# Kernel tuning notes

Hardware: AMD Instinct MI355X
Metric: run time of the kernel (lower is better)

Reference implementation:

```python
import jax, jax.numpy as jnp
import numpy as np

B = 256        # batch size
D = 256        # feature dim
N = 100000     # memory bank size (num pseudo classes)
TEMP = 0.07    # SCT_Memory temperature


def setup_inputs() -> dict:
    key = jax.random.key(0)
    k1, k2, k3 = jax.random.split(key, 3)
    inputs = jax.random.normal(k1, (B, D), dtype=jnp.float32)
    # ReID features are L2-normalized before hitting the memory
    inputs = inputs / jnp.linalg.norm(inputs, axis=1, keepdims=True)
    indexes = jax.random.randint(k2, (B,), 0, N, dtype=jnp.int32)
    features = jax.random.normal(k3, (N, D), dtype=jnp.float32)
    features = features / jnp.linalg.norm(features, axis=1, keepdims=True)
    return {"inputs": inputs, "indexes": indexes, "features": features,
            "momentum": 0.2}


def reference(inputs, indexes, features, momentum):
    # ExemplarMemory.forward: outputs = inputs.mm(features.t())
    # SCT_Memory then scales by 1/temp to form cluster_score.
    out = jnp.matmul(inputs, features.T)  # [B, N]
    return out / TEMP
```

## Files before the change

kernel.cpp:

```cpp
#include <hip/hip_runtime.h>
#include <hip/hip_bf16.h>


typedef __attribute__((ext_vector_type(8))) __bf16 bf16x8;
typedef __attribute__((ext_vector_type(4))) float  floatx4;
typedef __attribute__((ext_vector_type(4))) unsigned int uint4v;

#define NB 100000
#define KD 256
#define BN 64
#define NTILES 1563
#define GRID 256
#define LDS_STRIDE 132

union FragCast { uint4v u; bf16x8 f; };

__device__ __forceinline__ unsigned pk(float a, float b) {
  __hip_bfloat162 h = __float22bfloat162_rn(float2{a, b});
  union { __hip_bfloat162 h2; unsigned u; } c; c.h2 = h; return c.u;
}

__global__ __launch_bounds__(1024, 4)
void sct_gemm(const float* __restrict__ inputs,
              const float* __restrict__ features,
              float* __restrict__ out) {
  __shared__ unsigned lds[BN * LDS_STRIDE];

  const int tid  = threadIdx.x;
  const int ws   = tid >> 6;
  const int lane = tid & 63;
  const int quad = lane >> 4;
  const int l16  = lane & 15;

  const int b = blockIdx.x;
  const int ntiles = (NTILES - b + GRID - 1) / GRID;

  const int srow0 = tid >> 5,            sck0 = tid & 31;
  const int srow1 = (1024 + tid) >> 5,   sck1 = tid & 31;

  float4 pf0a, pf0b, pf1a, pf1b;
  {
    const int n0 = b * BN;
    pf0a = pf0b = pf1a = pf1b = make_float4(0.f, 0.f, 0.f, 0.f);
    if (n0 + srow0 < NB) {
      const float4* p = (const float4*)(features + (size_t)(n0 + srow0) * KD + sck0 * 8);
      pf0a = p[0]; pf0b = p[1];
    }
    if (n0 + srow1 < NB) {
      const float4* p = (const float4*)(features + (size_t)(n0 + srow1) * KD + sck1 * 8);
      pf1a = p[0]; pf1b = p[1];
    }
  }

  const float scale = 1.0f / 0.07f;
  bf16x8 afrag[8];
  {
    const float* arow = inputs + (ws * 16 + l16) * KD + quad * 8;
    #pragma unroll
    for (int t = 0; t < 8; ++t) {
      const float4* p = (const float4*)(arow + t * 32);
      const float4 a0 = p[0], a1 = p[1];
      FragCast fc;
      fc.u.x = pk(a0.x * scale, a0.y * scale);
      fc.u.y = pk(a0.z * scale, a0.w * scale);
      fc.u.z = pk(a1.x * scale, a1.y * scale);
      fc.u.w = pk(a1.z * scale, a1.w * scale);
      afrag[t] = fc.f;
    }
  }

  const unsigned obase = (unsigned)((ws * 16 + quad * 4) * NB + l16);

  for (int it = 0; it < ntiles; ++it) {
    const int n0 = (b + it * GRID) * BN;

    __syncthreads();

    {
      uint4v w;
      w.x = pk(pf0a.x, pf0a.y); w.y = pk(pf0a.z, pf0a.w);
      w.z = pk(pf0b.x, pf0b.y); w.w = pk(pf0b.z, pf0b.w);
      *(uint4v*)&lds[srow0 * LDS_STRIDE + sck0 * 4] = w;
      w.x = pk(pf1a.x, pf1a.y); w.y = pk(pf1a.z, pf1a.w);
      w.z = pk(pf1b.x, pf1b.y); w.w = pk(pf1b.z, pf1b.w);
      *(uint4v*)&lds[srow1 * LDS_STRIDE + sck1 * 4] = w;
    }
    __syncthreads();

    if (it + 1 < ntiles) {
      const int nn0 = (b + (it + 1) * GRID) * BN;
      pf0a = pf0b = pf1a = pf1b = make_float4(0.f, 0.f, 0.f, 0.f);
      if (nn0 + srow0 < NB) {
        const float4* p = (const float4*)(features + (size_t)(nn0 + srow0) * KD + sck0 * 8);
        pf0a = p[0]; pf0b = p[1];
      }
      if (nn0 + srow1 < NB) {
        const float4* p = (const float4*)(features + (size_t)(nn0 + srow1) * KD + sck1 * 8);
        pf1a = p[0]; pf1b = p[1];
      }
    }

    floatx4 acc[4];
    #pragma unroll
    for (int nt = 0; nt < 4; ++nt) acc[nt] = floatx4{0.f, 0.f, 0.f, 0.f};

    #pragma unroll
    for (int t = 0; t < 8; ++t) {
      #pragma unroll
      for (int nt = 0; nt < 4; ++nt) {
        FragCast fc;
        fc.u = *(const uint4v*)&lds[(nt * 16 + l16) * LDS_STRIDE + t * 16 + quad * 4];
        acc[nt] = __builtin_amdgcn_mfma_f32_16x16x32_bf16(afrag[t], fc.f, acc[nt], 0, 0, 0);
      }
    }

    #pragma unroll
    for (int nt = 0; nt < 4; ++nt) {
      const int n = n0 + nt * 16 + l16;
      if (n < NB) {
        const unsigned col = obase + (unsigned)(n0 + nt * 16);
        #pragma unroll
        for (int r = 0; r < 4; ++r)
          out[col + (unsigned)(r * NB)] = acc[nt][r];
      }
    }
  }
}

extern "C" void kernel_launch(void* const* d_in, const int* in_sizes, int n_in,
                              void* d_out, int out_size, void* d_ws, size_t ws_size,
                              hipStream_t stream) {
  const float* inputs   = (const float*)d_in[0];
  const float* features = (const float*)d_in[2];
  float* out = (float*)d_out;

  sct_gemm<<<GRID, 1024, 0, stream>>>(inputs, features, out);
}
```

Measured before the change: 200.2 us.

## Stage A in swizzled LDS, stream B straight from global per wave

Moves the scaled bf16 input matrix (half of the batch rows per block) into XOR-swizzled LDS. Each wave now loads its own 16-row feature slice directly from global into MFMA fragments, with no LDS staging of features and no per-tile block barriers. The grid doubles to 512 blocks, each wave group handles 16-column tasks strided across the bank, and launch bounds are raised to 8. This removes the syncthreads and the LDS round trip for B, but each feature row is now read from global twice (once per batch half) and the direct loads have no explicit prefetch.

```diff
diff --git a/kernel.cpp b/kernel.cpp
--- a/kernel.cpp
+++ b/kernel.cpp
@@ -6,12 +6,11 @@
 typedef __attribute__((ext_vector_type(4))) float  floatx4;
 typedef __attribute__((ext_vector_type(4))) unsigned int uint4v;
 
-#define NB 100000
-#define KD 256
-#define BN 64
-#define NTILES 1563
-#define GRID 256
-#define LDS_STRIDE 132
+#define NB    100000
+#define KD    256
+#define NSUB  6250
+#define NGRP  512
+#define GRIDB 512
 
 union FragCast { uint4v u; bf16x8 f; };
 
@@ -20,110 +19,73 @@
   union { __hip_bfloat162 h2; unsigned u; } c; c.h2 = h; return c.u;
 }
 
-__global__ __launch_bounds__(1024, 4)
+__global__ __launch_bounds__(1024, 8)
 void sct_gemm(const float* __restrict__ inputs,
               const float* __restrict__ features,
               float* __restrict__ out) {
-  __shared__ unsigned lds[BN * LDS_STRIDE];
+  __shared__ unsigned ldsA[128 * 128];
 
   const int tid  = threadIdx.x;
-  const int ws   = tid >> 6;
+  const int b    = blockIdx.x;
+  const int h    = b & 1;
+  const int wv   = tid >> 6;
   const int lane = tid & 63;
   const int quad = lane >> 4;
   const int l16  = lane & 15;
+  const float scale = 1.0f / 0.07f;
 
-  const int b = blockIdx.x;
-  const int ntiles = (NTILES - b + GRID - 1) / GRID;
+  #pragma unroll
+  for (int i = 0; i < 4; ++i) {
+    const int c  = i * 1024 + tid;
+    const int r  = c >> 5;
+    const int ck = c & 31;
+    const float4* p = (const float4*)(inputs + (size_t)(h * 128 + r) * KD + ck * 8);
+    const float4 a0 = p[0], a1 = p[1];
+    uint4v w;
+    w.x = pk(a0.x * scale, a0.y * scale);
+    w.y = pk(a0.z * scale, a0.w * scale);
+    w.z = pk(a1.x * scale, a1.y * scale);
+    w.w = pk(a1.z * scale, a1.w * scale);
+    *(uint4v*)&ldsA[r * 128 + ((ck * 4) ^ ((r & 7) * 16))] = w;
+  }
+  __syncthreads();
 
-  const int srow0 = tid >> 5,            sck0 = tid & 31;
-  const int srow1 = (1024 + tid) >> 5,   sck1 = tid & 31;
+  const int mb = wv & 7;
+  const int g  = ((b >> 1) << 1) + (wv >> 3);
 
-  float4 pf0a, pf0b, pf1a, pf1b;
-  {
-    const int n0 = b * BN;
-    pf0a = pf0b = pf1a = pf1b = make_float4(0.f, 0.f, 0.f, 0.f);
-    if (n0 + srow0 < NB) {
-      const float4* p = (const float4*)(features + (size_t)(n0 + srow0) * KD + sck0 * 8);
-      pf0a = p[0]; pf0b = p[1];
-    }
-    if (n0 + srow1 < NB) {
-      const float4* p = (const float4*)(features + (size_t)(n0 + srow1) * KD + sck1 * 8);
-      pf1a = p[0]; pf1b = p[1];
-    }
-  }
+  const unsigned aBase = (unsigned)((mb * 16 + l16) * 128 + quad * 4);
+  const unsigned aSwz  = (unsigned)((l16 & 7) * 16);
 
-  const float scale = 1.0f / 0.07f;
-  bf16x8 afrag[8];
-  {
-    const float* arow = inputs + (ws * 16 + l16) * KD + quad * 8;
-    #pragma unroll
-    for (int t = 0; t < 8; ++t) {
-      const float4* p = (const float4*)(arow + t * 32);
-      const float4 a0 = p[0], a1 = p[1];
-      FragCast fc;
-      fc.u.x = pk(a0.x * scale, a0.y * scale);
-      fc.u.y = pk(a0.z * scale, a0.w * scale);
-      fc.u.z = pk(a1.x * scale, a1.y * scale);
-      fc.u.w = pk(a1.z * scale, a1.w * scale);
-      afrag[t] = fc.f;
-    }
-  }
+  const int mrow = h * 128 + mb * 16 + quad * 4;
+  float* outp = out + (size_t)mrow * NB + l16;
 
-  const unsigned obase = (unsigned)((ws * 16 + quad * 4) * NB + l16);
+  const int ntasks = (NSUB - g + NGRP - 1) / NGRP;
+  const float* featp = features + (size_t)(g * 16 + l16) * KD;
 
-  for (int it = 0; it < ntiles; ++it) {
-    const int n0 = (b + it * GRID) * BN;
-
-    __syncthreads();
-
-    {
-      uint4v w;
-      w.x = pk(pf0a.x, pf0a.y); w.y = pk(pf0a.z, pf0a.w);
-      w.z = pk(pf0b.x, pf0b.y); w.w = pk(pf0b.z, pf0b.w);
-      *(uint4v*)&lds[srow0 * LDS_STRIDE + sck0 * 4] = w;
-      w.x = pk(pf1a.x, pf1a.y); w.y = pk(pf1a.z, pf1a.w);
-      w.z = pk(pf1b.x, pf1b.y); w.w = pk(pf1b.z, pf1b.w);
-      *(uint4v*)&lds[srow1 * LDS_STRIDE + sck1 * 4] = w;
-    }
-    __syncthreads();
-
-    if (it + 1 < ntiles) {
-      const int nn0 = (b + (it + 1) * GRID) * BN;
-      pf0a = pf0b = pf1a = pf1b = make_float4(0.f, 0.f, 0.f, 0.f);
-      if (nn0 + srow0 < NB) {
-        const float4* p = (const float4*)(features + (size_t)(nn0 + srow0) * KD + sck0 * 8);
-        pf0a = p[0]; pf0b = p[1];
-      }
-      if (nn0 + srow1 < NB) {
-        const float4* p = (const float4*)(features + (size_t)(nn0 + srow1) * KD + sck1 * 8);
-        pf1a = p[0]; pf1b = p[1];
-      }
-    }
-
-    floatx4 acc[4];
-    #pragma unroll
-    for (int nt = 0; nt < 4; ++nt) acc[nt] = floatx4{0.f, 0.f, 0.f, 0.f};
+  for (int it = 0; it < ntasks; ++it) {
+    floatx4 acc = {0.f, 0.f, 0.f, 0.f};
 
     #pragma unroll
     for (int t = 0; t < 8; ++t) {
-      #pragma unroll
-      for (int nt = 0; nt < 4; ++nt) {
-        FragCast fc;
-        fc.u = *(const uint4v*)&lds[(nt * 16 + l16) * LDS_STRIDE + t * 16 + quad * 4];
-        acc[nt] = __builtin_amdgcn_mfma_f32_16x16x32_bf16(afrag[t], fc.f, acc[nt], 0, 0, 0);
-      }
+      const float4* pB = (const float4*)(featp + t * 32 + quad * 8);
+      const float4 b0 = pB[0], b1 = pB[1];
+      FragCast bf;
+      bf.u.x = pk(b0.x, b0.y); bf.u.y = pk(b0.z, b0.w);
+      bf.u.z = pk(b1.x, b1.y); bf.u.w = pk(b1.z, b1.w);
+
+      FragCast af;
+      af.u = *(const uint4v*)&ldsA[aBase + (((unsigned)(t * 16)) ^ aSwz)];
+
+      acc = __builtin_amdgcn_mfma_f32_16x16x32_bf16(af.f, bf.f, acc, 0, 0, 0);
     }
 
+    const int n0 = (g + it * NGRP) * 16;
+    float* o = outp + n0;
     #pragma unroll
-    for (int nt = 0; nt < 4; ++nt) {
-      const int n = n0 + nt * 16 + l16;
-      if (n < NB) {
-        const unsigned col = obase + (unsigned)(n0 + nt * 16);
-        #pragma unroll
-        for (int r = 0; r < 4; ++r)
-          out[col + (unsigned)(r * NB)] = acc[nt][r];
-      }
-    }
+    for (int r = 0; r < 4; ++r)
+      o[(size_t)r * NB] = acc[r];
+
+    featp += (size_t)NGRP * 16 * KD;
   }
 }
 
@@ -134,5 +96,5 @@
   const float* features = (const float*)d_in[2];
   float* out = (float*)d_out;
 
-  sct_gemm<<<GRID, 1024, 0, stream>>>(inputs, features, out);
+  sct_gemm<<<GRIDB, 1024, 0, stream>>>(inputs, features, out);
 }
```

After: 339.0 us. 1.69x slower.

## Replace persistent prefetching loop with one-tile-per-block grid split across M halves

Applied to the files above, without the earlier changes.

Drops the persistent 256-block kernel, which looped over N tiles with register prefetch, and launches 2*1563 blocks of 512 threads. Each block handles one 64-column feature tile for half of the 256 batch rows. This gives many more independent blocks so the hardware can overlap loads and stores across them, replacing the explicit software prefetch. In exchange, each feature tile is loaded and converted twice (once per M half), the A fragments are reloaded per block, and the per-tile prefetch overlap is lost.

```diff
diff --git a/kernel.cpp b/kernel.cpp
--- a/kernel.cpp
+++ b/kernel.cpp
@@ -9,8 +9,7 @@
 #define NB 100000
 #define KD 256
 #define BN 64
-#define NTILES 1563
-#define GRID 256
+#define NT 1563
 #define LDS_STRIDE 132
 
 union FragCast { uint4v u; bf16x8 f; };
@@ -20,42 +19,43 @@
   union { __hip_bfloat162 h2; unsigned u; } c; c.h2 = h; return c.u;
 }
 
-__global__ __launch_bounds__(1024, 4)
+__global__ __launch_bounds__(512, 8)
 void sct_gemm(const float* __restrict__ inputs,
               const float* __restrict__ features,
               float* __restrict__ out) {
-  __shared__ unsigned lds[BN * LDS_STRIDE];
+  __shared__ unsigned ldsB[BN * LDS_STRIDE];
 
-  const int tid  = threadIdx.x;
-  const int ws   = tid >> 6;
+  const int tid = threadIdx.x;
+  const int b   = blockIdx.x;
+  const int mh  = b & 1;
+  const int n0  = (b >> 1) * BN;
+
+  const int wv   = tid >> 6;
   const int lane = tid & 63;
   const int quad = lane >> 4;
   const int l16  = lane & 15;
 
-  const int b = blockIdx.x;
-  const int ntiles = (NTILES - b + GRID - 1) / GRID;
-
-  const int srow0 = tid >> 5,            sck0 = tid & 31;
-  const int srow1 = (1024 + tid) >> 5,   sck1 = tid & 31;
-
-  float4 pf0a, pf0b, pf1a, pf1b;
-  {
-    const int n0 = b * BN;
-    pf0a = pf0b = pf1a = pf1b = make_float4(0.f, 0.f, 0.f, 0.f);
-    if (n0 + srow0 < NB) {
-      const float4* p = (const float4*)(features + (size_t)(n0 + srow0) * KD + sck0 * 8);
-      pf0a = p[0]; pf0b = p[1];
+  #pragma unroll
+  for (int i = 0; i < 4; ++i) {
+    const int c  = i * 512 + tid;
+    const int r  = c >> 5;
+    const int ck = c & 31;
+    const int n  = n0 + r;
+    float4 f0 = make_float4(0.f, 0.f, 0.f, 0.f), f1 = f0;
+    if (n < NB) {
+      const float4* p = (const float4*)(features + (size_t)n * KD + ck * 8);
+      f0 = p[0]; f1 = p[1];
     }
-    if (n0 + srow1 < NB) {
-      const float4* p = (const float4*)(features + (size_t)(n0 + srow1) * KD + sck1 * 8);
-      pf1a = p[0]; pf1b = p[1];
-    }
+    uint4v w;
+    w.x = pk(f0.x, f0.y); w.y = pk(f0.z, f0.w);
+    w.z = pk(f1.x, f1.y); w.w = pk(f1.z, f1.w);
+    *(uint4v*)&ldsB[r * LDS_STRIDE + ck * 4] = w;
   }
 
   const float scale = 1.0f / 0.07f;
   bf16x8 afrag[8];
   {
-    const float* arow = inputs + (ws * 16 + l16) * KD + quad * 8;
+    const float* arow = inputs + (size_t)(mh * 128 + wv * 16 + l16) * KD + quad * 8;
     #pragma unroll
     for (int t = 0; t < 8; ++t) {
       const float4* p = (const float4*)(arow + t * 32);
@@ -69,60 +69,30 @@
     }
   }
 
-  const unsigned obase = (unsigned)((ws * 16 + quad * 4) * NB + l16);
+  __syncthreads();
 
-  for (int it = 0; it < ntiles; ++it) {
-    const int n0 = (b + it * GRID) * BN;
+  floatx4 acc[4];
+  #pragma unroll
+  for (int nt = 0; nt < 4; ++nt) acc[nt] = floatx4{0.f, 0.f, 0.f, 0.f};
 
-    __syncthreads();
-
-    {
-      uint4v w;
-      w.x = pk(pf0a.x, pf0a.y); w.y = pk(pf0a.z, pf0a.w);
-      w.z = pk(pf0b.x, pf0b.y); w.w = pk(pf0b.z, pf0b.w);
-      *(uint4v*)&lds[srow0 * LDS_STRIDE + sck0 * 4] = w;
-      w.x = pk(pf1a.x, pf1a.y); w.y = pk(pf1a.z, pf1a.w);
-      w.z = pk(pf1b.x, pf1b.y); w.w = pk(pf1b.z, pf1b.w);
-      *(uint4v*)&lds[srow1 * LDS_STRIDE + sck1 * 4] = w;
-    }
-    __syncthreads();
-
-    if (it + 1 < ntiles) {
-      const int nn0 = (b + (it + 1) * GRID) * BN;
-      pf0a = pf0b = pf1a = pf1b = make_float4(0.f, 0.f, 0.f, 0.f);
-      if (nn0 + srow0 < NB) {
-        const float4* p = (const float4*)(features + (size_t)(nn0 + srow0) * KD + sck0 * 8);
-        pf0a = p[0]; pf0b = p[1];
-      }
-      if (nn0 + srow1 < NB) {
-        const float4* p = (const float4*)(features + (size_t)(nn0 + srow1) * KD + sck1 * 8);
-        pf1a = p[0]; pf1b = p[1];
-      }
-    }
-
-    floatx4 acc[4];
-    #pragma unroll
-    for (int nt = 0; nt < 4; ++nt) acc[nt] = floatx4{0.f, 0.f, 0.f, 0.f};
-
-    #pragma unroll
-    for (int t = 0; t < 8; ++t) {
-      #pragma unroll
-      for (int nt = 0; nt < 4; ++nt) {
-        FragCast fc;
-        fc.u = *(const uint4v*)&lds[(nt * 16 + l16) * LDS_STRIDE + t * 16 + quad * 4];
-        acc[nt] = __builtin_amdgcn_mfma_f32_16x16x32_bf16(afrag[t], fc.f, acc[nt], 0, 0, 0);
-      }
-    }
-
+  #pragma unroll
+  for (int t = 0; t < 8; ++t) {
     #pragma unroll
     for (int nt = 0; nt < 4; ++nt) {
-      const int n = n0 + nt * 16 + l16;
-      if (n < NB) {
-        const unsigned col = obase + (unsigned)(n0 + nt * 16);
-        #pragma unroll
-        for (int r = 0; r < 4; ++r)
-          out[col + (unsigned)(r * NB)] = acc[nt][r];
-      }
+      FragCast fc;
+      fc.u = *(const uint4v*)&ldsB[(nt * 16 + l16) * LDS_STRIDE + t * 16 + quad * 4];
+      acc[nt] = __builtin_amdgcn_mfma_f32_16x16x32_bf16(afrag[t], fc.f, acc[nt], 0, 0, 0);
+    }
+  }
+
+  const int mbase = mh * 128 + wv * 16 + quad * 4;
+  #pragma unroll
+  for (int nt = 0; nt < 4; ++nt) {
+    const int n = n0 + nt * 16 + l16;
+    if (n < NB) {
+      #pragma unroll
+      for (int r = 0; r < 4; ++r)
+        out[(size_t)(mbase + r) * NB + n] = acc[nt][r];
     }
   }
 }
@@ -134,5 +104,5 @@
   const float* features = (const float*)d_in[2];
   float* out = (float*)d_out;
 
-  sct_gemm<<<GRID, 1024, 0, stream>>>(inputs, features, out);
+  sct_gemm<<<2 * NT, 512, 0, stream>>>(inputs, features, out);
 }
```

Result: slower. 222.1 us (+10.9%).
